# Kernel tuning notes

Hardware: AMD Instinct MI355X
Metric: run time of the kernel (lower is better)

## Reference

```python
import jax, jax.numpy as jnp
from jax import lax
import numpy as np

B, T, C, V, E, H, OC = 1024, 32, 14, 21128, 200, 50, 8


def gru(x, Wih, Whh, bih, bhh):
    # x: [N, T, E] -> hiddens [N, T, H]; torch nn.GRU gate order (r, z, n)
    Hd = Whh.shape[1]
    xp = jnp.einsum('nte,ge->ntg', x, Wih) + bih  # [N, T, 3H]
    h0 = jnp.zeros((x.shape[0], Hd), x.dtype)

    def step(h, xt):
        gh = h @ Whh.T + bhh
        r = jax.nn.sigmoid(xt[:, :Hd] + gh[:, :Hd])
        z = jax.nn.sigmoid(xt[:, Hd:2 * Hd] + gh[:, Hd:2 * Hd])
        n = jnp.tanh(xt[:, 2 * Hd:] + r * gh[:, 2 * Hd:])
        h_new = (1.0 - z) * n + z * h
        return h_new, h_new

    _, hs = lax.scan(step, h0, jnp.swapaxes(xp, 0, 1))
    return jnp.swapaxes(hs, 0, 1)


def setup_inputs():
    key = jax.random.key(0)
    ks = jax.random.split(key, 32)
    s = 0.1
    inp = {
        'contexts_indices': jax.random.randint(ks[0], (B, T), 0, V),
        'candidates_indices': jax.random.randint(ks[1], (B, C, T), 0, V),
        'y_dev': jax.random.uniform(ks[2], (B, C), dtype=jnp.float32),
        'emb': jax.random.normal(ks[3], (V, E), dtype=jnp.float32),
        'A': jax.random.normal(ks[4], (H, H), dtype=jnp.float32) * s,
        'Wih_c': jax.random.normal(ks[5], (3 * H, E), dtype=jnp.float32) * s,
        'Whh_c': jax.random.normal(ks[6], (3 * H, H), dtype=jnp.float32) * s,
        'bih_c': jnp.zeros((3 * H,), jnp.float32),
        'bhh_c': jnp.zeros((3 * H,), jnp.float32),
        'Wih_r': jax.random.normal(ks[7], (3 * H, E), dtype=jnp.float32) * s,
        'Whh_r': jax.random.normal(ks[8], (3 * H, H), dtype=jnp.float32) * s,
        'bih_r': jnp.zeros((3 * H,), jnp.float32),
        'bhh_r': jnp.zeros((3 * H,), jnp.float32),
        'conv_w': jax.random.normal(ks[9], (OC, 2, 3, 3), dtype=jnp.float32) * s,
        'Wih2': jax.random.normal(ks[10], (3 * H, OC * 10 * 10), dtype=jnp.float32) * s,
        'Whh2': jax.random.normal(ks[11], (3 * H, H), dtype=jnp.float32) * s,
        'bih2': jnp.zeros((3 * H,), jnp.float32),
        'bhh2': jnp.zeros((3 * H,), jnp.float32),
        'fc1_w': jax.random.normal(ks[12], (100, C * H), dtype=jnp.float32) * s,
        'fc1_b': jnp.zeros((100,), jnp.float32),
        'fc2_w': jax.random.normal(ks[13], (C, 100), dtype=jnp.float32) * s,
        'fc2_b': jnp.zeros((C,), jnp.float32),
    }
    return inp


def reference(contexts_indices, candidates_indices, y_dev, emb, A,
              Wih_c, Whh_c, bih_c, bhh_c, Wih_r, Whh_r, bih_r, bhh_r,
              conv_w, Wih2, Whh2, bih2, bhh2, fc1_w, fc1_b, fc2_w, fc2_b):
    b = contexts_indices.shape[0]
    ctx = contexts_indices[:, None, :]                      # [B,1,T]
    ctx_emb = emb[ctx]                                      # [B,1,T,E] (dropout = identity in eval)
    cand_emb = emb[candidates_indices]                      # [B,C,T,E]

    ctx_h = gru(ctx_emb.reshape(-1, T, E), Wih_c, Whh_c, bih_c, bhh_c).reshape(b, 1, T, H)
    cand_h = gru(cand_emb.reshape(-1, T, E), Wih_r, Whh_r, bih_r, bhh_r).reshape(b, C, T, H)

    M1 = jnp.einsum('btph,bcqh->btcpq', ctx_emb, cand_emb)  # [B,1,C,T,T]
    ctx_hA = jnp.einsum('btij,jk->btik', ctx_h, A)
    M2 = jnp.einsum('btph,bcqh->btcpq', ctx_hA, cand_h)

    # faithful to torch: stack on dim 2 then row-major view(-1, 2, T, T)
    M = jnp.stack([M1, M2], axis=2).reshape(-1, 2, T, T)    # [B*C, 2, T, T]

    conv = lax.conv_general_dilated(M, conv_w, (1, 1), 'VALID',
                                    dimension_numbers=('NCHW', 'OIHW', 'NCHW'))  # [B*C, OC, 30, 30]
    pooled = lax.reduce_window(conv, -jnp.inf, lax.max,
                               (1, 1, 3, 3), (1, 1, 3, 3), 'VALID')              # [B*C, OC, 10, 10]

    feats = pooled.reshape(b, C, OC * 10 * 10)              # [B, C, 800]
    Hs = gru(feats, Wih2, Whh2, bih2, bhh2)                 # [B, C, H]
    flat = Hs.reshape(b, -1)                                # [B, C*H]

    hid = jax.nn.relu(flat @ fc1_w.T + fc1_b)
    log_probs = jax.nn.log_softmax(hid @ fc2_w.T + fc2_b, axis=-1)  # softmax then log
    kl = jnp.where(y_dev > 0, y_dev * (jnp.log(y_dev) - log_probs), 0.0)
    return jnp.mean(kl)
```

## Files before the change

### kernel.cpp

```cpp
#include <hip/hip_runtime.h>
#include <math.h>

typedef unsigned short u16;
typedef short s16;
typedef u16 u16x8 __attribute__((ext_vector_type(8)));
typedef s16 short8v __attribute__((ext_vector_type(8)));
typedef float f32x4 __attribute__((ext_vector_type(4)));

__device__ __forceinline__ float b2f(u16 u) {
    return __uint_as_float(((unsigned)u) << 16);
}
__device__ __forceinline__ u16 f2b(float f) {
    unsigned u = __float_as_uint(f);
    unsigned r = (u + 0x7FFFu + ((u >> 16) & 1u)) >> 16;
    return (u16)r;
}

__global__ __launch_bounds__(256) void k_cvt_all(
    const float* __restrict__ emb, u16* __restrict__ embh,
    const float* __restrict__ wcf, u16* __restrict__ wch,
    const float* __restrict__ wrf, u16* __restrict__ wrh,
    const float* __restrict__ w2f, u16* __restrict__ w2h)
{
    long j = (long)blockIdx.x * 256 + threadIdx.x;
    if (j < 1056400) {
        float4 v = ((const float4*)emb)[j];
        *(ushort4*)(embh + j * 4) = make_ushort4(f2b(v.x), f2b(v.y), f2b(v.z), f2b(v.w));
        return;
    }
    j -= 1056400;
    if (j < 7500) {
        float4 v = ((const float4*)wcf)[j];
        *(ushort4*)(wch + j * 4) = make_ushort4(f2b(v.x), f2b(v.y), f2b(v.z), f2b(v.w));
        return;
    }
    j -= 7500;
    if (j < 7500) {
        float4 v = ((const float4*)wrf)[j];
        *(ushort4*)(wrh + j * 4) = make_ushort4(f2b(v.x), f2b(v.y), f2b(v.z), f2b(v.w));
        return;
    }
    j -= 7500;
    if (j < 120000) {
        int jj = (int)(j / 800), k = (int)(j % 800);
        int p = k >> 3, oc = k & 7;
        w2h[jj * 800 + k] = f2b(w2f[jj * 800 + oc * 100 + p]);
    }
}

__global__ __launch_bounds__(256) void k_projmm2(
    const u16* __restrict__ embh, const u16* __restrict__ wc,
    const u16* __restrict__ wr, const float* __restrict__ bc,
    const float* __restrict__ br, u16* __restrict__ outc,
    u16* __restrict__ outr, int V)
{
    __shared__ s16 Ab[2048];
    __shared__ s16 Bb[2560];
    __shared__ float bhL[160];
    const int t = threadIdx.x;
    const int w = t >> 6, l = t & 63, lg = l >> 4, lr = l & 15;
    int id = blockIdx.x;
    const int half = (id >= 662) ? 1 : 0;
    id -= half * 662;
    const u16* wh = half ? wr : wc;
    const float* bias = half ? br : bc;
    u16* outp = half ? outr : outc;
    const int mb = id >> 1, nb = id & 1;
    const long rowbase = (long)mb * 64;
    const int colbase = nb * 80;
    if (t < 160) bhL[t] = (t < 150) ? bias[t] : 0.f;

    f32x4 acc[5];
#pragma unroll
    for (int i = 0; i < 5; ++i) acc[i] = (f32x4){0,0,0,0};

    for (int ch = 0; ch < 7; ++ch) {
        __syncthreads();
        {
            int kc = t >> 6, row = t & 63;
            long grow = rowbase + row; if (grow >= V) grow = V - 1;
            int k0 = ch * 32 + kc * 8;
            short8v v = {0,0,0,0,0,0,0,0};
            if (k0 < 200) v = *(const short8v*)(embh + grow * 200 + k0);
            *(short8v*)&Ab[t * 8] = v;
        }
        for (int it = t; it < 320; it += 256) {
            int kc = it / 80, col = it % 80;
            int gcol = colbase + col;
            int k0 = ch * 32 + kc * 8;
            short8v v = {0,0,0,0,0,0,0,0};
            if (gcol < 150 && k0 < 200)
                v = *(const short8v*)(wh + (size_t)gcol * 200 + k0);
            *(short8v*)&Bb[it * 8] = v;
        }
        __syncthreads();
        short8v a = *(short8v*)&Ab[(lg * 64 + w * 16 + lr) * 8];
#pragma unroll
        for (int ct = 0; ct < 5; ++ct) {
            short8v bv = *(short8v*)&Bb[(lg * 80 + ct * 16 + lr) * 8];
            acc[ct] = __builtin_amdgcn_mfma_f32_16x16x32_bf16(a, bv, acc[ct], 0, 0, 0);
        }
    }
#pragma unroll
    for (int ct = 0; ct < 5; ++ct) {
        int gcol = colbase + ct * 16 + lr;
        if (gcol < 150) {
#pragma unroll
            for (int rr = 0; rr < 4; ++rr) {
                long row = rowbase + w * 16 + lg * 4 + rr;
                outp[row * 152 + gcol] = f2b(acc[ct][rr] + bhL[gcol]);
            }
        }
    }
}

template<int MODE, int SEQS>
__device__ __forceinline__ void gru_body(
    char* sm, const void* __restrict__ xp_, const int* __restrict__ idx,
    const float* __restrict__ Whh, const float* __restrict__ bhh,
    void* __restrict__ hs_, int T, long blk)
{
    s16*   hbuf = (s16*)sm;
    float* ghL  = (float*)(sm + 2048);
    float* hL   = (float*)(sm + 2048 + SEQS * 640);
    float* bhL  = (float*)(sm + 2048 + SEQS * 848);
    u16*   xraw = (u16*)(sm + 2048 + SEQS * 848 + 608);
    const int t = threadIdx.x;
    const int w = t >> 6, l = t & 63, lg = l >> 4, lr = l & 15;
    constexpr int HST = (MODE == 2) ? 56 : 50;
    constexpr int XROW = SEQS * 152;
    u16*   xbH = xraw;
    float* xbF = (float*)xraw;

    for (int li = t; li < 1024; li += 256) hbuf[li] = 0;
    for (int e = t; e < SEQS * 52; e += 256) hL[e] = 0.f;
    if (t < 152) bhL[t] = (t < 150) ? bhh[t] : 0.f;

    const int te_0 = (w * 3     > 9) ? 9 : w * 3;
    const int te_1 = (w * 3 + 1 > 9) ? 9 : w * 3 + 1;
    const int te_2 = (w * 3 + 2 > 9) ? 9 : w * 3 + 2;
    short8v B00 = {0,0,0,0,0,0,0,0}, B01 = B00, B10 = B00, B11 = B00, B20 = B00, B21 = B00;
    {
        int cols[3] = { te_0 * 16 + lr, te_1 * 16 + lr, te_2 * 16 + lr };
        short8v* frg[6] = { &B00, &B01, &B10, &B11, &B20, &B21 };
#pragma unroll
        for (int ti = 0; ti < 3; ++ti) {
            int col = cols[ti];
            if (col < 150) {
#pragma unroll
                for (int s = 0; s < 2; ++s) {
                    short8v v = {0,0,0,0,0,0,0,0};
#pragma unroll
                    for (int e = 0; e < 8; ++e) {
                        int k = (s * 4 + lg) * 8 + e;
                        if (k < 50) v[e] = (s16)f2b(Whh[col * 50 + k]);
                    }
                    *frg[ti * 2 + s] = v;
                }
            }
        }
    }

    const long seqbase = blk * SEQS;
    const float* xpf = (const float*)xp_;
    const u16*   xph = (const u16*)xp_;
    float* hsf = (float*)hs_;
    u16*   hsh = (u16*)hs_;

    const int rA = (MODE == 2) ? t / 19 : t / 38;
    const int oA = (MODE == 2) ? (t % 19) * 8 : (t % 38) * 4;
    const int rB = (MODE == 2) ? (t + 256) / 19 : (t + 256) / 38;
    const int oB = (MODE == 2) ? ((t + 256) % 19) * 8 : ((t + 256) % 38) * 4;
    const bool actA = (MODE == 2) ? (t < SEQS * 19) : true;
    const bool hasB = (MODE == 2) ? (t + 256 < SEQS * 19) : (t + 256 < SEQS * 38);

    auto rowbase = [&](int rr, int stp) -> size_t {
        long r = seqbase + rr;
        long src = (MODE == 0) ? (r * T + stp) : (long)idx[r * T + stp];
        return (size_t)src * 152;
    };

    if (MODE == 2) {
        if (actA) *(u16x8*)&xbH[rA * 152 + oA] = *(const u16x8*)(xph + rowbase(rA, 0) + oA);
        if (hasB) *(u16x8*)&xbH[rB * 152 + oB] = *(const u16x8*)(xph + rowbase(rB, 0) + oB);
    } else {
        *(float4*)&xbF[rA * 152 + oA] = *(const float4*)(xpf + rowbase(rA, 0) + oA);
        if (hasB)
            *(float4*)&xbF[rB * 152 + oB] = *(const float4*)(xpf + rowbase(rB, 0) + oB);
    }
    __syncthreads();

    for (int st = 0; st < T; ++st) {
        const int cur = st & 1;
        u16x8 pfh0, pfh1;
        float4 pf0, pf1;
        if (st + 1 < T) {
            if (MODE == 2) {
                if (actA) pfh0 = *(const u16x8*)(xph + rowbase(rA, st + 1) + oA);
                if (hasB) pfh1 = *(const u16x8*)(xph + rowbase(rB, st + 1) + oB);
            } else {
                pf0 = *(const float4*)(xpf + rowbase(rA, st + 1) + oA);
                if (hasB) pf1 = *(const float4*)(xpf + rowbase(rB, st + 1) + oB);
            }
        }
        short8v a0 = *(short8v*)&hbuf[((0 + lg) * 16 + lr) * 8];
        short8v a1 = *(short8v*)&hbuf[((4 + lg) * 16 + lr) * 8];
        f32x4 c0 = {0,0,0,0}, c1 = {0,0,0,0}, c2 = {0,0,0,0};
        c0 = __builtin_amdgcn_mfma_f32_16x16x32_bf16(a0, B00, c0, 0, 0, 0);
        c0 = __builtin_amdgcn_mfma_f32_16x16x32_bf16(a1, B01, c0, 0, 0, 0);
        c1 = __builtin_amdgcn_mfma_f32_16x16x32_bf16(a0, B10, c1, 0, 0, 0);
        c1 = __builtin_amdgcn_mfma_f32_16x16x32_bf16(a1, B11, c1, 0, 0, 0);
        c2 = __builtin_amdgcn_mfma_f32_16x16x32_bf16(a0, B20, c2, 0, 0, 0);
        c2 = __builtin_amdgcn_mfma_f32_16x16x32_bf16(a1, B21, c2, 0, 0, 0);
        if (lg * 4 < SEQS) {
            int col0 = te_0 * 16 + lr, col1 = te_1 * 16 + lr, col2 = te_2 * 16 + lr;
            if (col0 < 150) {
#pragma unroll
                for (int r = 0; r < 4; ++r) ghL[(lg * 4 + r) * 160 + col0] = c0[r] + bhL[col0];
            }
            if (col1 < 150) {
#pragma unroll
                for (int r = 0; r < 4; ++r) ghL[(lg * 4 + r) * 160 + col1] = c1[r] + bhL[col1];
            }
            if (col2 < 150) {
#pragma unroll
                for (int r = 0; r < 4; ++r) ghL[(lg * 4 + r) * 160 + col2] = c2[r] + bhL[col2];
            }
        }
        __syncthreads();
        if (st + 1 < T) {
            if (MODE == 2) {
                if (actA) *(u16x8*)&xbH[(cur ^ 1) * XROW + rA * 152 + oA] = pfh0;
                if (hasB) *(u16x8*)&xbH[(cur ^ 1) * XROW + rB * 152 + oB] = pfh1;
            } else {
                *(float4*)&xbF[(cur ^ 1) * XROW + rA * 152 + oA] = pf0;
                if (hasB) *(float4*)&xbF[(cur ^ 1) * XROW + rB * 152 + oB] = pf1;
            }
        }
        for (int item = t; item < SEQS * 50; item += 256) {
            int ss = item / 50, hh = item % 50;
            float xv0, xv1, xv2;
            if (MODE == 2) {
                const u16* xr = &xbH[cur * XROW + ss * 152];
                xv0 = b2f(xr[hh]); xv1 = b2f(xr[50 + hh]); xv2 = b2f(xr[100 + hh]);
            } else {
                const float* xr = &xbF[cur * XROW + ss * 152];
                xv0 = xr[hh]; xv1 = xr[50 + hh]; xv2 = xr[100 + hh];
            }
            float vr  = xv0 + ghL[ss * 160 + hh];
            float vz  = xv1 + ghL[ss * 160 + 50 + hh];
            float ghn = ghL[ss * 160 + 100 + hh];
            float rg = 1.f / (1.f + __expf(-vr));
            float zg = 1.f / (1.f + __expf(-vz));
            float a = xv2 + rg * ghn;
            a = fminf(fmaxf(a, -15.f), 15.f);
            float e2 = __expf(-2.f * a);
            float nn2 = (1.f - e2) / (1.f + e2);
            float hn = (1.f - zg) * nn2 + zg * hL[ss * 52 + hh];
            hL[ss * 52 + hh] = hn;
            hbuf[((hh >> 3) * 16 + ss) * 8 + (hh & 7)] = (s16)f2b(hn);
            size_t ofs = ((size_t)(seqbase + ss) * T + st) * HST + hh;
            if (MODE == 2) hsh[ofs] = f2b(hn); else hsf[ofs] = hn;
        }
        __syncthreads();
    }
}

__device__ __forceinline__ void conv_pool_epi2(
    s16* pool, short8v Bc, const int* dlt,
    u16* __restrict__ feats, long nl, f32x4 cacc0, f32x4 cacc1)
{
    u16* Mb    = (u16*)pool;
    u16* convL = (u16*)pool + 2184;
    const int t = threadIdx.x;
    const int w = t >> 6, l = t & 63, lg = l >> 4, lr = l & 15;
    const int job0 = w * 2, job1 = w * 2 + 1;
    const int ch0 = job0 >> 2, rt0 = (job0 >> 1) & 1, ct0 = job0 & 1;
    const int ch1 = job1 >> 2, rt1 = (job1 >> 1) & 1, ct1 = job1 & 1;

    __syncthreads();
#pragma unroll
    for (int rr = 0; rr < 4; ++rr) {
        Mb[ch0 * 1092 + (rt0 * 16 + lg * 4 + rr) * 33 + ct0 * 16 + lr] = f2b(cacc0[rr]);
        Mb[ch1 * 1092 + (rt1 * 16 + lg * 4 + rr) * 33 + ct1 * 16 + lr] = f2b(cacc1[rr]);
    }
    __syncthreads();

    for (int tile = w; tile < 29; tile += 4) {
        int m = tile * 16 + lr;
        int cy = m / 30, cx = m - cy * 30;
        int base = cy * 33 + cx;
        short8v a;
#pragma unroll
        for (int e = 0; e < 8; ++e) a[e] = (s16)Mb[base + dlt[e]];
        f32x4 c = {0,0,0,0};
        c = __builtin_amdgcn_mfma_f32_16x16x32_bf16(a, Bc, c, 0, 0, 0);
        if (lr < 8) {
#pragma unroll
            for (int rr = 0; rr < 4; ++rr)
                convL[(tile * 16 + lg * 4 + rr) * 8 + lr] = f2b(c[rr]);
        }
    }
    __syncthreads();
    if (t < 50) {
        int py = t / 10, px = t % 10;
        int m0 = (3 * py) * 30 + 3 * px;
        float mx[8];
#pragma unroll
        for (int c = 0; c < 8; ++c) mx[c] = -1e30f;
#pragma unroll
        for (int dy = 0; dy < 3; ++dy)
#pragma unroll
            for (int dx = 0; dx < 3; ++dx) {
                u16x8 v = *(u16x8*)&convL[(m0 + dy * 30 + dx) * 8];
#pragma unroll
                for (int c = 0; c < 8; ++c) mx[c] = fmaxf(mx[c], b2f(v[c]));
            }
        u16x8 o;
#pragma unroll
        for (int c = 0; c < 8; ++c) o[c] = f2b(mx[c]);
        *(u16x8*)(feats + nl * 800 + t * 8) = o;
    }
    __syncthreads();
    for (int tile = 28 + w; tile < 57; tile += 4) {
        int m = tile * 16 + lr;
        int cy = m / 30, cx = m - cy * 30;
        int base = cy * 33 + cx;
        short8v a;
#pragma unroll
        for (int e = 0; e < 8; ++e) a[e] = (s16)Mb[base + dlt[e]];
        f32x4 c = {0,0,0,0};
        c = __builtin_amdgcn_mfma_f32_16x16x32_bf16(a, Bc, c, 0, 0, 0);
        if (lr < 8) {
#pragma unroll
            for (int rr = 0; rr < 4; ++rr)
                convL[(tile * 16 + lg * 4 + rr - 448) * 8 + lr] = f2b(c[rr]);
        }
    }
    __syncthreads();
    if (t < 50) {
        int py = 5 + t / 10, px = t % 10;
        int m0 = (3 * py) * 30 + 3 * px - 448;
        float mx[8];
#pragma unroll
        for (int c = 0; c < 8; ++c) mx[c] = -1e30f;
#pragma unroll
        for (int dy = 0; dy < 3; ++dy)
#pragma unroll
            for (int dx = 0; dx < 3; ++dx) {
                u16x8 v = *(u16x8*)&convL[(m0 + dy * 30 + dx) * 8];
#pragma unroll
                for (int c = 0; c < 8; ++c) mx[c] = fmaxf(mx[c], b2f(v[c]));
            }
        u16x8 o;
#pragma unroll
        for (int c = 0; c < 8; ++c) o[c] = f2b(mx[c]);
        *(u16x8*)(feats + nl * 800 + (50 + t) * 8) = o;
    }
    __syncthreads();
}

__device__ __forceinline__ void m1_super(
    char* sm, const u16* __restrict__ embh, const int* __restrict__ ctx_idx,
    const int* __restrict__ cand_idx, const float* __restrict__ conv_w,
    u16* __restrict__ feats, int m)
{
    s16* ctxL = (s16*)sm;
    s16* canL = (s16*)sm + 6600;
    float* wL = (float*)(sm + 25680);
    int* ci = (int*)(sm + 26256);
    int* qi = (int*)(sm + 26384);
    const int t = threadIdx.x;
    const int xcd = m & 7, bq = m >> 3;
    const int b = bq * 8 + xcd;
    const int w = t >> 6, l = t & 63, lg = l >> 4, lr = l & 15;

    if (t < 144) wL[t] = conv_w[t];
    if (t >= 160 && t < 192) ci[t - 160] = ctx_idx[b * 32 + (t - 160)];
    __syncthreads();

    for (int it = t; it < 800; it += 256) {
        int kc = it >> 5, row = it & 31;
        *(short8v*)&ctxL[(kc * 33 + row) * 8] =
            *(const short8v*)(embh + (size_t)ci[row] * 200 + kc * 8);
    }
    short8v Bc = {0,0,0,0,0,0,0,0};
    int dlt[8];
#pragma unroll
    for (int e = 0; e < 8; ++e) {
        int s = lg * 8 + e;
        if (s < 18) {
            int ch = s / 9, r9 = s % 9, ky = r9 / 3, kx = r9 % 3;
            dlt[e] = ch * 1092 + ky * 33 + kx;
            if (lr < 8) Bc[e] = (s16)f2b(wL[lr * 18 + s]);
        } else dlt[e] = 0;
    }

    const int job0 = w * 2, job1 = w * 2 + 1;
    const int ch0 = job0 >> 2, rt0 = (job0 >> 1) & 1, ct0 = job0 & 1;
    const int ch1 = job1 >> 2, rt1 = (job1 >> 1) & 1, ct1 = job1 & 1;

    for (int r = 0; r < 7; ++r) {
        if (t < 64)
            qi[t] = cand_idx[((long)b * 14 + 2 * r + (t >> 5)) * 32 + (t & 31)];
        f32x4 cacc0 = {0,0,0,0}, cacc1 = {0,0,0,0};
#pragma unroll
        for (int cnk = 0; cnk < 3; ++cnk) {
            const int kcbase = (cnk == 0) ? 0 : (cnk == 1 ? 12 : 20);
            const int kccnt  = (cnk == 0) ? 12 : 8;
            const int scnt   = (cnk == 0) ? 3 : 2;
            __syncthreads();
            for (int it = t; it < kccnt * 64; it += 256) {
                int kcl = it >> 6, col = it & 63;
                int kc = kcbase + kcl;
                short8v v = {0,0,0,0,0,0,0,0};
                if (kc < 25)
                    v = *(const short8v*)(embh + (size_t)qi[(col >> 5) * 32 + (col & 31)] * 200 + kc * 8);
                *(short8v*)&canL[(kcl * 65 + col) * 8] = v;
            }
            __syncthreads();
            for (int sl = 0; sl < scnt; ++sl) {
                int kcl = sl * 4 + lg;
                int kc = kcbase + kcl;
                short8v a0 = *(short8v*)&ctxL[(kc * 33 + rt0 * 16 + lr) * 8];
                short8v b0 = *(short8v*)&canL[(kcl * 65 + ch0 * 32 + ct0 * 16 + lr) * 8];
                short8v b1 = *(short8v*)&canL[(kcl * 65 + ch1 * 32 + ct1 * 16 + lr) * 8];
                cacc0 = __builtin_amdgcn_mfma_f32_16x16x32_bf16(a0, b0, cacc0, 0, 0, 0);
                short8v a1 = (rt0 == rt1) ? a0
                           : *(short8v*)&ctxL[(kc * 33 + rt1 * 16 + lr) * 8];
                cacc1 = __builtin_amdgcn_mfma_f32_16x16x32_bf16(a1, b1, cacc1, 0, 0, 0);
            }
        }
        conv_pool_epi2(canL, Bc, dlt, feats, (long)b * 14 + r, cacc0, cacc1);
    }
}

__global__ __launch_bounds__(256) void k_scan_m1(
    const u16* __restrict__ proj_ch, const u16* __restrict__ proj_rh,
    const int* __restrict__ ctx_idx, const int* __restrict__ cand_idx,
    const float* __restrict__ Whh_c, const float* __restrict__ Whh_r,
    const float* __restrict__ bhh_c, const float* __restrict__ bhh_r,
    u16* __restrict__ ctx_hh, u16* __restrict__ candh_h,
    const u16* __restrict__ embh, const float* __restrict__ conv_w,
    u16* __restrict__ feats)
{
    __shared__ long long smq[3330];
    char* sm = (char*)smq;
    const long bid = blockIdx.x;
    if (bid < 960) {
        const bool cand = (bid < 896);
        gru_body<2, 16>(sm,
                        cand ? (const void*)proj_rh : (const void*)proj_ch,
                        cand ? cand_idx : ctx_idx,
                        cand ? Whh_r : Whh_c,
                        cand ? bhh_r : bhh_c,
                        cand ? (void*)candh_h : (void*)ctx_hh,
                        32, cand ? bid : bid - 896);
    } else {
        m1_super(sm, embh, ctx_idx, cand_idx, conv_w, feats, (int)(bid - 960));
    }
}

__global__ __launch_bounds__(256) void k_m2conv(
    const u16* __restrict__ ctxA_h, const u16* __restrict__ candh_h,
    const float* __restrict__ conv_w, u16* __restrict__ feats)
{
    __shared__ long long smq[1640];
    char* sm = (char*)smq;
    s16* aL = (s16*)sm;
    s16* cL = (s16*)sm + 2112;
    float* wL = (float*)(sm + 12544);
    const int t = threadIdx.x;
    const int wg = blockIdx.x;
    const int xcd = wg & 7, q = wg >> 3;
    const int r7 = q % 7, bq = q / 7;
    const int b = bq * 8 + xcd;
    const long nl = (long)b * 14 + 7 + r7;
    const int w = t >> 6, l = t & 63, lg = l >> 4, lr = l & 15;

    if (t < 144) wL[t] = conv_w[t];

    f32x4 cacc0 = {0,0,0,0}, cacc1 = {0,0,0,0};
    const int job0 = w * 2, job1 = w * 2 + 1;
    const int ch0 = job0 >> 2, rt0 = (job0 >> 1) & 1, ct0 = job0 & 1;
    const int ch1 = job1 >> 2, rt1 = (job1 >> 1) & 1, ct1 = job1 & 1;

    const int c0 = 2 * r7;
    for (int it = t; it < 256; it += 256) {
        int kc = it >> 5, row = it & 31;
        short8v v = {0,0,0,0,0,0,0,0};
        if (kc < 7) {
            v = *(const short8v*)(ctxA_h + (size_t)(b * 32 + row) * 56 + kc * 8);
            if (kc == 6) { v[2] = 0; v[3] = 0; v[4] = 0; v[5] = 0; v[6] = 0; v[7] = 0; }
        }
        *(short8v*)&aL[(kc * 33 + row) * 8] = v;
    }
    for (int it = t; it < 512; it += 256) {
        int kc = it >> 6, col = it & 63;
        long row = ((long)b * 14 + c0 + (col >> 5)) * 32 + (col & 31);
        short8v v = {0,0,0,0,0,0,0,0};
        if (kc < 7) {
            v = *(const short8v*)(candh_h + (size_t)row * 56 + kc * 8);
            if (kc == 6) { v[2] = 0; v[3] = 0; v[4] = 0; v[5] = 0; v[6] = 0; v[7] = 0; }
        }
        *(short8v*)&cL[(kc * 65 + col) * 8] = v;
    }
    __syncthreads();

    short8v Bc = {0,0,0,0,0,0,0,0};
    int dlt[8];
#pragma unroll
    for (int e = 0; e < 8; ++e) {
        int s = lg * 8 + e;
        if (s < 18) {
            int ch = s / 9, r9 = s % 9, ky = r9 / 3, kx = r9 % 3;
            dlt[e] = ch * 1092 + ky * 33 + kx;
            if (lr < 8) Bc[e] = (s16)f2b(wL[lr * 18 + s]);
        } else dlt[e] = 0;
    }

#pragma unroll
    for (int sl = 0; sl < 2; ++sl) {
        int kcl = sl * 4 + lg;
        short8v a0 = *(short8v*)&aL[(kcl * 33 + rt0 * 16 + lr) * 8];
        short8v b0 = *(short8v*)&cL[(kcl * 65 + ch0 * 32 + ct0 * 16 + lr) * 8];
        short8v b1 = *(short8v*)&cL[(kcl * 65 + ch1 * 32 + ct1 * 16 + lr) * 8];
        cacc0 = __builtin_amdgcn_mfma_f32_16x16x32_bf16(a0, b0, cacc0, 0, 0, 0);
        short8v a1 = (rt0 == rt1) ? a0
                   : *(short8v*)&aL[(kcl * 33 + rt1 * 16 + lr) * 8];
        cacc1 = __builtin_amdgcn_mfma_f32_16x16x32_bf16(a1, b1, cacc1, 0, 0, 0);
    }
    conv_pool_epi2((s16*)sm, Bc, dlt, feats, nl, cacc0, cacc1);
}

__global__ __launch_bounds__(256) void k_scan2(
    const float* __restrict__ xp2, const float* __restrict__ Whh2,
    const float* __restrict__ bhh2, float* __restrict__ hs2)
{
    __shared__ long long smq[2396];
    gru_body<0, 8>((char*)smq, xp2, nullptr, Whh2, bhh2, hs2, 14, (long)blockIdx.x);
}

__global__ __launch_bounds__(256) void k_matA(
    const u16* __restrict__ inh, const float* __restrict__ A,
    u16* __restrict__ outh)
{
    __shared__ float AL[50 * 52];
    __shared__ float inL[32 * 52];
    const int t = threadIdx.x;
    for (int e = t; e < 2500; e += 256) AL[(e / 50) * 52 + (e % 50)] = A[e];
    const long rbase = (long)blockIdx.x * 32;
    for (int e = t; e < 1600; e += 256) {
        int r = e / 50, j = e % 50;
        inL[r * 52 + j] = b2f(inh[(rbase + r) * 56 + j]);
    }
    __syncthreads();
    for (int item = t; item < 1600; item += 256) {
        int r = item / 50, kk = item % 50;
        float acc = 0.f;
#pragma unroll 10
        for (int j = 0; j < 50; ++j)
            acc += inL[r * 52 + j] * AL[j * 52 + kk];
        outh[(rbase + r) * 56 + kk] = f2b(acc);
    }
}

__global__ __launch_bounds__(256) void k_xp2mm(
    const u16* __restrict__ feats, const u16* __restrict__ w2h,
    const float* __restrict__ bih2, float* __restrict__ out)
{
    __shared__ s16 Ab[2048];
    __shared__ s16 Bb[2560];
    __shared__ float bhL[160];
    const int t = threadIdx.x;
    const int w = t >> 6, l = t & 63, lg = l >> 4, lr = l & 15;
    const int mb = blockIdx.x >> 1, nb = blockIdx.x & 1;
    const long rowbase = (long)mb * 64;
    const int colbase = nb * 80;
    if (t < 160) bhL[t] = (t < 150) ? bih2[t] : 0.f;

    f32x4 acc[5];
#pragma unroll
    for (int i = 0; i < 5; ++i) acc[i] = (f32x4){0,0,0,0};

    for (int ch = 0; ch < 25; ++ch) {
        __syncthreads();
        {
            int kc = t >> 6, row = t & 63;
            *(short8v*)&Ab[t * 8] =
                *(const short8v*)(feats + (rowbase + row) * 800 + ch * 32 + kc * 8);
        }
        for (int it = t; it < 320; it += 256) {
            int kc = it / 80, col = it % 80;
            int gcol = colbase + col;
            short8v v = {0,0,0,0,0,0,0,0};
            if (gcol < 150)
                v = *(const short8v*)(w2h + (size_t)gcol * 800 + ch * 32 + kc * 8);
            *(short8v*)&Bb[it * 8] = v;
        }
        __syncthreads();
        short8v a = *(short8v*)&Ab[(lg * 64 + w * 16 + lr) * 8];
#pragma unroll
        for (int ct = 0; ct < 5; ++ct) {
            short8v bv = *(short8v*)&Bb[(lg * 80 + ct * 16 + lr) * 8];
            acc[ct] = __builtin_amdgcn_mfma_f32_16x16x32_bf16(a, bv, acc[ct], 0, 0, 0);
        }
    }
#pragma unroll
    for (int ct = 0; ct < 5; ++ct) {
        int gcol = colbase + ct * 16 + lr;
        if (gcol < 150) {
#pragma unroll
            for (int rr = 0; rr < 4; ++rr) {
                long row = rowbase + w * 16 + lg * 4 + rr;
                out[row * 152 + gcol] = acc[ct][rr] + bhL[gcol];
            }
        }
    }
}

__global__ __launch_bounds__(128) void k_head(
    const float* __restrict__ Hs, const float* __restrict__ w1,
    const float* __restrict__ b1, const float* __restrict__ w2,
    const float* __restrict__ b2, const float* __restrict__ y,
    float* __restrict__ partial)
{
    __shared__ float hr[700];
    __shared__ float hidL[100];
    const int t = threadIdx.x;
    const long b = blockIdx.x;
    for (int e = t; e < 700; e += 128) hr[e] = Hs[b * 700 + e];
    __syncthreads();
    if (t < 100) {
        float acc = b1[t];
        const float4* wp = (const float4*)(w1 + (size_t)t * 700);
        for (int k4 = 0; k4 < 175; ++k4) {
            float4 wv = wp[k4];
            float4 hv = *(float4*)&hr[k4 * 4];
            acc += wv.x * hv.x + wv.y * hv.y + wv.z * hv.z + wv.w * hv.w;
        }
        hidL[t] = fmaxf(acc, 0.f);
    }
    __syncthreads();
    if (t < 64) {
        float logit = -1e30f;
        if (t < 14) {
            logit = b2[t];
            for (int k = 0; k < 100; ++k) logit += hidL[k] * w2[t * 100 + k];
        }
        float m = logit;
        for (int off = 8; off; off >>= 1) m = fmaxf(m, __shfl_xor(m, off, 16));
        float ex = (t < 14) ? __expf(logit - m) : 0.f;
        float se = ex;
        for (int off = 8; off; off >>= 1) se += __shfl_xor(se, off, 16);
        float kl = 0.f;
        if (t < 14) {
            float lp = logit - m - __logf(se);
            float yv = y[b * 14 + t];
            kl = (yv > 0.f) ? yv * (__logf(yv) - lp) : 0.f;
        }
        for (int off = 8; off; off >>= 1) kl += __shfl_xor(kl, off, 16);
        if (t == 0) partial[b] = kl;
    }
}

__global__ __launch_bounds__(256) void k_reduce(
    const float* __restrict__ partial, float* __restrict__ out)
{
    __shared__ float sm[256];
    const int t = threadIdx.x;
    sm[t] = partial[t] + partial[t + 256] + partial[t + 512] + partial[t + 768];
    __syncthreads();
    for (int off = 128; off; off >>= 1) {
        if (t < off) sm[t] += sm[t + off];
        __syncthreads();
    }
    if (t == 0) out[0] = sm[0] * (1.f / 14336.f);
}

extern "C" void kernel_launch(void* const* d_in, const int* in_sizes, int n_in,
                              void* d_out, int out_size, void* d_ws, size_t ws_size,
                              hipStream_t stream)
{
    const int*   ctx_idx  = (const int*)d_in[0];
    const int*   cand_idx = (const int*)d_in[1];
    const float* y_dev    = (const float*)d_in[2];
    const float* emb      = (const float*)d_in[3];
    const float* A        = (const float*)d_in[4];
    const float* Wih_c    = (const float*)d_in[5];
    const float* Whh_c    = (const float*)d_in[6];
    const float* bih_c    = (const float*)d_in[7];
    const float* bhh_c    = (const float*)d_in[8];
    const float* Wih_r    = (const float*)d_in[9];
    const float* Whh_r    = (const float*)d_in[10];
    const float* bih_r    = (const float*)d_in[11];
    const float* bhh_r    = (const float*)d_in[12];
    const float* conv_w   = (const float*)d_in[13];
    const float* Wih2     = (const float*)d_in[14];
    const float* Whh2     = (const float*)d_in[15];
    const float* bih2     = (const float*)d_in[16];
    const float* bhh2     = (const float*)d_in[17];
    const float* fc1_w    = (const float*)d_in[18];
    const float* fc1_b    = (const float*)d_in[19];
    const float* fc2_w    = (const float*)d_in[20];
    const float* fc2_b    = (const float*)d_in[21];

    float* ws = (float*)d_ws;
    u16*   embh    = (u16*)ws;
    u16*   proj_ch = (u16*)(ws + 2112800);
    u16*   proj_rh = (u16*)(ws + 3722784);
    u16*   ctx_hh  = (u16*)(ws + 5332768);
    u16*   ctxA_h  = (u16*)(ws + 6250272);
    u16*   candh_h = (u16*)(ws + 7167776);
    u16*   feats_h = (u16*)(ws + 20012832);
    u16*   w2h     = (u16*)(ws + 25747232);
    u16*   wch     = (u16*)(ws + 25807232);
    u16*   wrh     = (u16*)(ws + 25822232);
    float* xp2     = ws + 25837232;
    float* hs2     = ws + 28016304;
    float* part    = ws + 28733104;

    k_cvt_all <<<4654, 256, 0, stream>>>(emb, embh, Wih_c, wch, Wih_r, wrh,
                                         Wih2, w2h);
    k_projmm2 <<<1324, 256, 0, stream>>>(embh, wch, wrh, bih_c, bih_r,
                                         proj_ch, proj_rh, 21128);
    k_scan_m1 <<<1984, 256, 0, stream>>>(proj_ch, proj_rh, ctx_idx, cand_idx,
                                         Whh_c, Whh_r, bhh_c, bhh_r,
                                         ctx_hh, candh_h, embh, conv_w, feats_h);
    k_matA <<<1024, 256, 0, stream>>>(ctx_hh, A, ctxA_h);
    k_m2conv <<<7168, 256, 0, stream>>>(ctxA_h, candh_h, conv_w, feats_h);
    k_xp2mm <<<448, 256, 0, stream>>>(feats_h, w2h, bih2, xp2);
    k_scan2 <<<128, 256, 0, stream>>>(xp2, Whh2, bhh2, hs2);
    k_head <<<1024, 128, 0, stream>>>(hs2, fc1_w, fc1_b, fc2_w, fc2_b, y_dev, part);
    k_reduce <<<1, 256, 0, stream>>>(part, (float*)d_out);
}
```

Measured before the change: 317.0 us.

## Split M1 super-blocks into one workgroup per candidate pair with single-pass conv epilogue

Each M1 block previously looped over 7 candidate pairs for one batch element. Now each workgroup handles a single pair, so the grid grows from 1024 to 7168 M1 blocks. The context embeddings are chunk-loaded alongside the candidate chunks, which shrinks LDS use. The conv/pool epilogue becomes a single pass over all 57 tiles with 100 pooling threads instead of two halves. This aims to raise parallelism and occupancy and to overlap better with the GRU scan blocks, at the cost of re-gathering context embeddings and conv weights once per pair.

```diff
diff --git a/kernel.cpp b/kernel.cpp
--- a/kernel.cpp
+++ b/kernel.cpp
@@ -266,12 +266,13 @@
     }
 }
 
-__device__ __forceinline__ void conv_pool_epi2(
-    s16* pool, short8v Bc, const int* dlt,
-    u16* __restrict__ feats, long nl, f32x4 cacc0, f32x4 cacc1)
-{
-    u16* Mb    = (u16*)pool;
-    u16* convL = (u16*)pool + 2184;
+__device__ __forceinline__ void conv_pool_epi(
+    char* sm, u16* __restrict__ feats, long nl, f32x4 cacc0, f32x4 cacc1)
+{
+    s16* pool16 = (s16*)sm;
+    float* wL = (float*)(sm + 18960);
+    u16* Mb    = (u16*)pool16;
+    u16* convL = (u16*)pool16 + 2184;
     const int t = threadIdx.x;
     const int w = t >> 6, l = t & 63, lg = l >> 4, lr = l & 15;
     const int job0 = w * 2, job1 = w * 2 + 1;
@@ -284,106 +285,7 @@
         Mb[ch0 * 1092 + (rt0 * 16 + lg * 4 + rr) * 33 + ct0 * 16 + lr] = f2b(cacc0[rr]);
         Mb[ch1 * 1092 + (rt1 * 16 + lg * 4 + rr) * 33 + ct1 * 16 + lr] = f2b(cacc1[rr]);
     }
-    __syncthreads();
-
-    for (int tile = w; tile < 29; tile += 4) {
-        int m = tile * 16 + lr;
-        int cy = m / 30, cx = m - cy * 30;
-        int base = cy * 33 + cx;
-        short8v a;
-#pragma unroll
-        for (int e = 0; e < 8; ++e) a[e] = (s16)Mb[base + dlt[e]];
-        f32x4 c = {0,0,0,0};
-        c = __builtin_amdgcn_mfma_f32_16x16x32_bf16(a, Bc, c, 0, 0, 0);
-        if (lr < 8) {
-#pragma unroll
-            for (int rr = 0; rr < 4; ++rr)
-                convL[(tile * 16 + lg * 4 + rr) * 8 + lr] = f2b(c[rr]);
-        }
-    }
-    __syncthreads();
-    if (t < 50) {
-        int py = t / 10, px = t % 10;
-        int m0 = (3 * py) * 30 + 3 * px;
-        float mx[8];
-#pragma unroll
-        for (int c = 0; c < 8; ++c) mx[c] = -1e30f;
-#pragma unroll
-        for (int dy = 0; dy < 3; ++dy)
-#pragma unroll
-            for (int dx = 0; dx < 3; ++dx) {
-                u16x8 v = *(u16x8*)&convL[(m0 + dy * 30 + dx) * 8];
-#pragma unroll
-                for (int c = 0; c < 8; ++c) mx[c] = fmaxf(mx[c], b2f(v[c]));
-            }
-        u16x8 o;
-#pragma unroll
-        for (int c = 0; c < 8; ++c) o[c] = f2b(mx[c]);
-        *(u16x8*)(feats + nl * 800 + t * 8) = o;
-    }
-    __syncthreads();
-    for (int tile = 28 + w; tile < 57; tile += 4) {
-        int m = tile * 16 + lr;
-        int cy = m / 30, cx = m - cy * 30;
-        int base = cy * 33 + cx;
-        short8v a;
-#pragma unroll
-        for (int e = 0; e < 8; ++e) a[e] = (s16)Mb[base + dlt[e]];
-        f32x4 c = {0,0,0,0};
-        c = __builtin_amdgcn_mfma_f32_16x16x32_bf16(a, Bc, c, 0, 0, 0);
-        if (lr < 8) {
-#pragma unroll
-            for (int rr = 0; rr < 4; ++rr)
-                convL[(tile * 16 + lg * 4 + rr - 448) * 8 + lr] = f2b(c[rr]);
-        }
-    }
-    __syncthreads();
-    if (t < 50) {
-        int py = 5 + t / 10, px = t % 10;
-        int m0 = (3 * py) * 30 + 3 * px - 448;
-        float mx[8];
-#pragma unroll
-        for (int c = 0; c < 8; ++c) mx[c] = -1e30f;
-#pragma unroll
-        for (int dy = 0; dy < 3; ++dy)
-#pragma unroll
-            for (int dx = 0; dx < 3; ++dx) {
-                u16x8 v = *(u16x8*)&convL[(m0 + dy * 30 + dx) * 8];
-#pragma unroll
-                for (int c = 0; c < 8; ++c) mx[c] = fmaxf(mx[c], b2f(v[c]));
-            }
-        u16x8 o;
-#pragma unroll
-        for (int c = 0; c < 8; ++c) o[c] = f2b(mx[c]);
-        *(u16x8*)(feats + nl * 800 + (50 + t) * 8) = o;
-    }
-    __syncthreads();
-}
-
-__device__ __forceinline__ void m1_super(
-    char* sm, const u16* __restrict__ embh, const int* __restrict__ ctx_idx,
-    const int* __restrict__ cand_idx, const float* __restrict__ conv_w,
-    u16* __restrict__ feats, int m)
-{
-    s16* ctxL = (s16*)sm;
-    s16* canL = (s16*)sm + 6600;
-    float* wL = (float*)(sm + 25680);
-    int* ci = (int*)(sm + 26256);
-    int* qi = (int*)(sm + 26384);
-    const int t = threadIdx.x;
-    const int xcd = m & 7, bq = m >> 3;
-    const int b = bq * 8 + xcd;
-    const int w = t >> 6, l = t & 63, lg = l >> 4, lr = l & 15;
-
-    if (t < 144) wL[t] = conv_w[t];
-    if (t >= 160 && t < 192) ci[t - 160] = ctx_idx[b * 32 + (t - 160)];
-    __syncthreads();
-
-    for (int it = t; it < 800; it += 256) {
-        int kc = it >> 5, row = it & 31;
-        *(short8v*)&ctxL[(kc * 33 + row) * 8] =
-            *(const short8v*)(embh + (size_t)ci[row] * 200 + kc * 8);
-    }
+
     short8v Bc = {0,0,0,0,0,0,0,0};
     int dlt[8];
 #pragma unroll
@@ -395,44 +297,205 @@
             if (lr < 8) Bc[e] = (s16)f2b(wL[lr * 18 + s]);
         } else dlt[e] = 0;
     }
-
+    __syncthreads();
+
+    for (int tile = w; tile < 57; tile += 4) {
+        int m = tile * 16 + lr;
+        int cy = m / 30, cx = m - cy * 30;
+        int base = cy * 33 + cx;
+        short8v a;
+#pragma unroll
+        for (int e = 0; e < 8; ++e) a[e] = (s16)Mb[base + dlt[e]];
+        f32x4 c = {0,0,0,0};
+        c = __builtin_amdgcn_mfma_f32_16x16x32_bf16(a, Bc, c, 0, 0, 0);
+        if (lr < 8) {
+#pragma unroll
+            for (int rr = 0; rr < 4; ++rr)
+                convL[(tile * 16 + lg * 4 + rr) * 8 + lr] = f2b(c[rr]);
+        }
+    }
+    __syncthreads();
+
+    if (t < 100) {
+        int py = t / 10, px = t % 10;
+        int m0 = (3 * py) * 30 + 3 * px;
+        float mx[8];
+#pragma unroll
+        for (int c = 0; c < 8; ++c) mx[c] = -1e30f;
+#pragma unroll
+        for (int dy = 0; dy < 3; ++dy)
+#pragma unroll
+            for (int dx = 0; dx < 3; ++dx) {
+                u16x8 v = *(u16x8*)&convL[(m0 + dy * 30 + dx) * 8];
+#pragma unroll
+                for (int c = 0; c < 8; ++c) mx[c] = fmaxf(mx[c], b2f(v[c]));
+            }
+        u16x8 o;
+#pragma unroll
+        for (int c = 0; c < 8; ++c) o[c] = f2b(mx[c]);
+        *(u16x8*)(feats + nl * 800 + t * 8) = o;
+    }
+}
+
+__device__ __forceinline__ void conv_pool_epi2(
+    s16* pool, short8v Bc, const int* dlt,
+    u16* __restrict__ feats, long nl, f32x4 cacc0, f32x4 cacc1)
+{
+    u16* Mb    = (u16*)pool;
+    u16* convL = (u16*)pool + 2184;
+    const int t = threadIdx.x;
+    const int w = t >> 6, l = t & 63, lg = l >> 4, lr = l & 15;
     const int job0 = w * 2, job1 = w * 2 + 1;
     const int ch0 = job0 >> 2, rt0 = (job0 >> 1) & 1, ct0 = job0 & 1;
     const int ch1 = job1 >> 2, rt1 = (job1 >> 1) & 1, ct1 = job1 & 1;
 
-    for (int r = 0; r < 7; ++r) {
-        if (t < 64)
-            qi[t] = cand_idx[((long)b * 14 + 2 * r + (t >> 5)) * 32 + (t & 31)];
-        f32x4 cacc0 = {0,0,0,0}, cacc1 = {0,0,0,0};
-#pragma unroll
-        for (int cnk = 0; cnk < 3; ++cnk) {
-            const int kcbase = (cnk == 0) ? 0 : (cnk == 1 ? 12 : 20);
-            const int kccnt  = (cnk == 0) ? 12 : 8;
-            const int scnt   = (cnk == 0) ? 3 : 2;
-            __syncthreads();
-            for (int it = t; it < kccnt * 64; it += 256) {
-                int kcl = it >> 6, col = it & 63;
-                int kc = kcbase + kcl;
-                short8v v = {0,0,0,0,0,0,0,0};
-                if (kc < 25)
-                    v = *(const short8v*)(embh + (size_t)qi[(col >> 5) * 32 + (col & 31)] * 200 + kc * 8);
-                *(short8v*)&canL[(kcl * 65 + col) * 8] = v;
-            }
-            __syncthreads();
-            for (int sl = 0; sl < scnt; ++sl) {
-                int kcl = sl * 4 + lg;
-                int kc = kcbase + kcl;
-                short8v a0 = *(short8v*)&ctxL[(kc * 33 + rt0 * 16 + lr) * 8];
-                short8v b0 = *(short8v*)&canL[(kcl * 65 + ch0 * 32 + ct0 * 16 + lr) * 8];
-                short8v b1 = *(short8v*)&canL[(kcl * 65 + ch1 * 32 + ct1 * 16 + lr) * 8];
-                cacc0 = __builtin_amdgcn_mfma_f32_16x16x32_bf16(a0, b0, cacc0, 0, 0, 0);
-                short8v a1 = (rt0 == rt1) ? a0
-                           : *(short8v*)&ctxL[(kc * 33 + rt1 * 16 + lr) * 8];
-                cacc1 = __builtin_amdgcn_mfma_f32_16x16x32_bf16(a1, b1, cacc1, 0, 0, 0);
-            }
-        }
-        conv_pool_epi2(canL, Bc, dlt, feats, (long)b * 14 + r, cacc0, cacc1);
-    }
+    __syncthreads();
+#pragma unroll
+    for (int rr = 0; rr < 4; ++rr) {
+        Mb[ch0 * 1092 + (rt0 * 16 + lg * 4 + rr) * 33 + ct0 * 16 + lr] = f2b(cacc0[rr]);
+        Mb[ch1 * 1092 + (rt1 * 16 + lg * 4 + rr) * 33 + ct1 * 16 + lr] = f2b(cacc1[rr]);
+    }
+    __syncthreads();
+
+    for (int tile = w; tile < 29; tile += 4) {
+        int m = tile * 16 + lr;
+        int cy = m / 30, cx = m - cy * 30;
+        int base = cy * 33 + cx;
+        short8v a;
+#pragma unroll
+        for (int e = 0; e < 8; ++e) a[e] = (s16)Mb[base + dlt[e]];
+        f32x4 c = {0,0,0,0};
+        c = __builtin_amdgcn_mfma_f32_16x16x32_bf16(a, Bc, c, 0, 0, 0);
+        if (lr < 8) {
+#pragma unroll
+            for (int rr = 0; rr < 4; ++rr)
+                convL[(tile * 16 + lg * 4 + rr) * 8 + lr] = f2b(c[rr]);
+        }
+    }
+    __syncthreads();
+    if (t < 50) {
+        int py = t / 10, px = t % 10;
+        int m0 = (3 * py) * 30 + 3 * px;
+        float mx[8];
+#pragma unroll
+        for (int c = 0; c < 8; ++c) mx[c] = -1e30f;
+#pragma unroll
+        for (int dy = 0; dy < 3; ++dy)
+#pragma unroll
+            for (int dx = 0; dx < 3; ++dx) {
+                u16x8 v = *(u16x8*)&convL[(m0 + dy * 30 + dx) * 8];
+#pragma unroll
+                for (int c = 0; c < 8; ++c) mx[c] = fmaxf(mx[c], b2f(v[c]));
+            }
+        u16x8 o;
+#pragma unroll
+        for (int c = 0; c < 8; ++c) o[c] = f2b(mx[c]);
+        *(u16x8*)(feats + nl * 800 + t * 8) = o;
+    }
+    __syncthreads();
+    for (int tile = 28 + w; tile < 57; tile += 4) {
+        int m = tile * 16 + lr;
+        int cy = m / 30, cx = m - cy * 30;
+        int base = cy * 33 + cx;
+        short8v a;
+#pragma unroll
+        for (int e = 0; e < 8; ++e) a[e] = (s16)Mb[base + dlt[e]];
+        f32x4 c = {0,0,0,0};
+        c = __builtin_amdgcn_mfma_f32_16x16x32_bf16(a, Bc, c, 0, 0, 0);
+        if (lr < 8) {
+#pragma unroll
+            for (int rr = 0; rr < 4; ++rr)
+                convL[(tile * 16 + lg * 4 + rr - 448) * 8 + lr] = f2b(c[rr]);
+        }
+    }
+    __syncthreads();
+    if (t < 50) {
+        int py = 5 + t / 10, px = t % 10;
+        int m0 = (3 * py) * 30 + 3 * px - 448;
+        float mx[8];
+#pragma unroll
+        for (int c = 0; c < 8; ++c) mx[c] = -1e30f;
+#pragma unroll
+        for (int dy = 0; dy < 3; ++dy)
+#pragma unroll
+            for (int dx = 0; dx < 3; ++dx) {
+                u16x8 v = *(u16x8*)&convL[(m0 + dy * 30 + dx) * 8];
+#pragma unroll
+                for (int c = 0; c < 8; ++c) mx[c] = fmaxf(mx[c], b2f(v[c]));
+            }
+        u16x8 o;
+#pragma unroll
+        for (int c = 0; c < 8; ++c) o[c] = f2b(mx[c]);
+        *(u16x8*)(feats + nl * 800 + (50 + t) * 8) = o;
+    }
+    __syncthreads();
+}
+
+__device__ __forceinline__ void m1_body(
+    char* sm, const u16* __restrict__ embh, const int* __restrict__ ctx_idx,
+    const int* __restrict__ cand_idx, const float* __restrict__ conv_w,
+    u16* __restrict__ feats, int wg)
+{
+    s16* pool16 = (s16*)sm;
+    float* wL = (float*)(sm + 18960);
+    int* ci = (int*)(sm + 19536);
+    int* qi = (int*)(sm + 19664);
+    const int t = threadIdx.x;
+    const int xcd = wg & 7, q = wg >> 3;
+    const int r = q % 7, bq = q / 7;
+    const int b = bq * 8 + xcd;
+    const long nl = (long)b * 14 + r;
+    const int w = t >> 6, l = t & 63, lg = l >> 4, lr = l & 15;
+
+    if (t < 144) wL[t] = conv_w[t];
+
+    f32x4 cacc0 = {0,0,0,0}, cacc1 = {0,0,0,0};
+    const int job0 = w * 2, job1 = w * 2 + 1;
+    const int ch0 = job0 >> 2, rt0 = (job0 >> 1) & 1, ct0 = job0 & 1;
+    const int ch1 = job1 >> 2, rt1 = (job1 >> 1) & 1, ct1 = job1 & 1;
+
+    const int c0 = 2 * r;
+    if (t < 32) ci[t] = ctx_idx[b * 32 + t];
+    else if (t < 96)
+        qi[((t - 32) >> 5) * 32 + (t & 31)] =
+            cand_idx[((long)b * 14 + c0 + ((t - 32) >> 5)) * 32 + (t & 31)];
+    __syncthreads();
+    s16* ctxL = pool16;
+    s16* canL = pool16 + 3168;
+#pragma unroll
+    for (int cnk = 0; cnk < 3; ++cnk) {
+        const int kcbase = (cnk == 0) ? 0 : (cnk == 1 ? 12 : 20);
+        const int kccnt  = (cnk == 0) ? 12 : 8;
+        const int scnt   = (cnk == 0) ? 3 : 2;
+        if (cnk) __syncthreads();
+        for (int it = t; it < kccnt * 32; it += 256) {
+            int kcl = it >> 5, row = it & 31;
+            int kc = kcbase + kcl;
+            short8v v = {0,0,0,0,0,0,0,0};
+            if (kc < 25) v = *(const short8v*)(embh + (size_t)ci[row] * 200 + kc * 8);
+            *(short8v*)&ctxL[(kcl * 33 + row) * 8] = v;
+        }
+        for (int it = t; it < kccnt * 64; it += 256) {
+            int kcl = it >> 6, col = it & 63;
+            int kc = kcbase + kcl;
+            short8v v = {0,0,0,0,0,0,0,0};
+            if (kc < 25)
+                v = *(const short8v*)(embh + (size_t)qi[(col >> 5) * 32 + (col & 31)] * 200 + kc * 8);
+            *(short8v*)&canL[(kcl * 65 + col) * 8] = v;
+        }
+        __syncthreads();
+        for (int sl = 0; sl < scnt; ++sl) {
+            int kcl = sl * 4 + lg;
+            short8v a0 = *(short8v*)&ctxL[(kcl * 33 + rt0 * 16 + lr) * 8];
+            short8v b0 = *(short8v*)&canL[(kcl * 65 + ch0 * 32 + ct0 * 16 + lr) * 8];
+            short8v b1 = *(short8v*)&canL[(kcl * 65 + ch1 * 32 + ct1 * 16 + lr) * 8];
+            cacc0 = __builtin_amdgcn_mfma_f32_16x16x32_bf16(a0, b0, cacc0, 0, 0, 0);
+            short8v a1 = (rt0 == rt1) ? a0
+                       : *(short8v*)&ctxL[(kcl * 33 + rt1 * 16 + lr) * 8];
+            cacc1 = __builtin_amdgcn_mfma_f32_16x16x32_bf16(a1, b1, cacc1, 0, 0, 0);
+        }
+    }
+    conv_pool_epi(sm, feats, nl, cacc0, cacc1);
 }
 
 __global__ __launch_bounds__(256) void k_scan_m1(
@@ -444,7 +507,7 @@
     const u16* __restrict__ embh, const float* __restrict__ conv_w,
     u16* __restrict__ feats)
 {
-    __shared__ long long smq[3330];
+    __shared__ long long smq[3244];
     char* sm = (char*)smq;
     const long bid = blockIdx.x;
     if (bid < 960) {
@@ -457,7 +520,7 @@
                         cand ? (void*)candh_h : (void*)ctx_hh,
                         32, cand ? bid : bid - 896);
     } else {
-        m1_super(sm, embh, ctx_idx, cand_idx, conv_w, feats, (int)(bid - 960));
+        m1_body(sm, embh, ctx_idx, cand_idx, conv_w, feats, (int)(bid - 960));
     }
 }
 
@@ -724,7 +787,7 @@
                                          Wih2, w2h);
     k_projmm2 <<<1324, 256, 0, stream>>>(embh, wch, wrh, bih_c, bih_r,
                                          proj_ch, proj_rh, 21128);
-    k_scan_m1 <<<1984, 256, 0, stream>>>(proj_ch, proj_rh, ctx_idx, cand_idx,
+    k_scan_m1 <<<8128, 256, 0, stream>>>(proj_ch, proj_rh, ctx_idx, cand_idx,
                                          Whh_c, Whh_r, bhh_c, bhh_r,
                                          ctx_hh, candh_h, embh, conv_w, feats_h);
     k_matA <<<1024, 256, 0, stream>>>(ctx_hh, A, ctxA_h);
```

After: 305.2 us (median of 2 runs). 1.04x faster.
